# Kernel tuning notes

Measured on AMD Instinct MI355X. Metric: run time of the kernel, lower is better.

## Reference

```python
import jax, jax.numpy as jnp
import numpy as np

N_VERTICES = 100000
N_JOINTS = 24
N_BETAS = 300
PARENTS = [0, 0, 0, 0, 1, 2, 3, 4, 5, 6, 7, 8, 9, 9, 9, 12, 13, 14, 16, 17, 18, 19, 20, 21]


def rodrigues(r):
    """r: [N,1,3] axis-angle -> [N,3,3] rotation matrices.

    Original adds N(0,1e-8) noise before the norm purely to avoid 0/0; we use a
    deterministic epsilon inside the sqrt instead (same math up to ~1e-8).
    """
    theta = jnp.sqrt(jnp.sum(r * r, axis=(1, 2), keepdims=True) + 1e-16)  # [N,1,1]
    r_hat = r / theta                                                      # [N,1,3]
    cos = jnp.cos(theta)
    sin = jnp.sin(theta)
    x, y, z = r_hat[:, 0, 0], r_hat[:, 0, 1], r_hat[:, 0, 2]
    zero = jnp.zeros_like(x)
    m = jnp.stack([zero, -z, y, z, zero, -x, -y, x, zero], axis=1).reshape(-1, 3, 3)
    dot = jnp.einsum('nia,nib->nab', r_hat, r_hat)  # outer product r_hat^T r_hat
    eye = jnp.eye(3, dtype=r.dtype)
    return cos * eye + (1.0 - cos) * dot + sin * m


def _with_zeros(R3, t):
    # [3,3],[3] -> [4,4] homogeneous transform
    top = jnp.concatenate([R3, t[:, None]], axis=1)              # [3,4]
    bottom = jnp.array([[0.0, 0.0, 0.0, 1.0]], dtype=R3.dtype)
    return jnp.concatenate([top, bottom], axis=0)


def smpl_forward(beta, pose, v_template, J_regressor, skin_weights, shapedirs, posedirs):
    dtype = v_template.dtype
    # shape blendshapes: [V,3,K] . [K] -> [V,3]
    v_shaped = jnp.einsum('vdk,k->vd', shapedirs, beta) + v_template
    J = J_regressor @ v_shaped                                   # [24,3]

    pose_cube = pose.reshape(-1, 1, 3)                           # [24,1,3]
    R_cube_big = rodrigues(pose_cube)                            # [24,3,3]

    # pose blendshapes
    lrotmin = (R_cube_big[1:] - jnp.eye(3, dtype=dtype)).reshape(-1)   # [207]
    v_posed = v_shaped + jnp.einsum('vdp,p->vd', posedirs, lrotmin)    # [V,3]

    # kinematic chain (fixed 24-step sequential dependency)
    Gs = [_with_zeros(R_cube_big[0], J[0])]
    for i in range(1, N_JOINTS):
        j = PARENTS[i]
        Gs.append(Gs[j] @ _with_zeros(R_cube_big[i], J[i] - J[j]))
    G = jnp.stack(Gs)                                            # [24,4,4]

    # remove rest-pose joint locations: G - pad(G @ [J;0])
    J_h = jnp.concatenate([J, jnp.zeros((N_JOINTS, 1), dtype=dtype)], axis=1)  # [24,4]
    RJ = jnp.einsum('jab,jb->ja', G, J_h)                        # [24,4]
    G = G - jnp.pad(RJ[:, :, None], ((0, 0), (0, 0), (3, 0)))    # subtract into last column

    # linear blend skinning
    T = jnp.einsum('vj,jab->vab', skin_weights, G)               # [V,4,4]
    rest_h = jnp.pad(v_posed, ((0, 0), (0, 1)), constant_values=1.0)  # [V,4]
    v = jnp.einsum('vab,vb->va', T, rest_h)                      # [V,4]
    return v[:, :3]


def setup_inputs() -> dict:
    key = jax.random.key(0)
    ks = jax.random.split(key, 7)
    beta = jax.random.normal(ks[0], (N_BETAS,), dtype=jnp.float32)
    pose = jax.random.normal(ks[1], (N_JOINTS * 3,), dtype=jnp.float32)
    v_template = jax.random.normal(ks[2], (N_VERTICES, 3), dtype=jnp.float32)
    # NonNegUnitSum(axis=1) constraints -> nonnegative rows summing to 1
    Jr = jax.random.uniform(ks[3], (N_JOINTS, N_VERTICES), dtype=jnp.float32)
    J_regressor = Jr / jnp.sum(Jr, axis=1, keepdims=True)
    w = jax.random.uniform(ks[4], (N_VERTICES, N_JOINTS), dtype=jnp.float32)
    skin_weights = w / jnp.sum(w, axis=1, keepdims=True)
    shapedirs = 0.01 * jax.random.normal(ks[5], (N_VERTICES, 3, N_BETAS), dtype=jnp.float32)
    posedirs = 0.01 * jax.random.normal(ks[6], (N_VERTICES, 3, (N_JOINTS - 1) * 9), dtype=jnp.float32)
    return {'beta': beta, 'pose': pose, 'v_template': v_template,
            'J_regressor': J_regressor, 'skin_weights': skin_weights,
            'shapedirs': shapedirs, 'posedirs': posedirs}


def reference(beta, pose, v_template, J_regressor, skin_weights, shapedirs, posedirs):
    return smpl_forward(beta, pose, v_template, J_regressor, skin_weights, shapedirs, posedirs)
```

## Files before the change

kernel.cpp:

```cpp
#include <hip/hip_runtime.h>
#include <math.h>

#define N_V 100000
#define N_J 24
#define N_BETAS 300
#define N_POSE 207
#define JSPLIT 25

typedef float f4 __attribute__((ext_vector_type(4)));

__constant__ int c_parents[N_J] = {0,0,0,0,1,2,3,4,5,6,7,8,9,9,9,12,13,14,16,17,18,19,20,21};

__global__ void k_rodrigues(const float* __restrict__ pose,
                            float* __restrict__ ws_R,
                            float* __restrict__ ws_lrot) {
    __shared__ float Rsh[N_J][9];
    int t = threadIdx.x;
    if (t < N_J) {
        float x = pose[t*3+0], y = pose[t*3+1], z = pose[t*3+2];
        float th = sqrtf(x*x + y*y + z*z + 1e-16f);
        float inv = 1.0f / th;
        float rx = x*inv, ry = y*inv, rz = z*inv;
        float c = cosf(th), s = sinf(th), o = 1.0f - c;
        float R[9];
        R[0] = c + o*rx*rx;      R[1] = o*rx*ry - s*rz;  R[2] = o*rx*rz + s*ry;
        R[3] = o*ry*rx + s*rz;   R[4] = c + o*ry*ry;     R[5] = o*ry*rz - s*rx;
        R[6] = o*rz*rx - s*ry;   R[7] = o*rz*ry + s*rx;  R[8] = c + o*rz*rz;
        #pragma unroll
        for (int i = 0; i < 9; ++i) { Rsh[t][i] = R[i]; ws_R[t*9+i] = R[i]; }
    }
    __syncthreads();
    for (int i = t; i < N_POSE; i += blockDim.x) {
        int j = i / 9 + 1, e = i % 9;
        float v = Rsh[j][e];
        if (e == 0 || e == 4 || e == 8) v -= 1.0f;
        ws_lrot[i] = v;
    }
}

__global__ __launch_bounds__(256) void k_vertex(
        const float* __restrict__ shapedirs, const float* __restrict__ posedirs,
        const float* __restrict__ v_template, const float* __restrict__ beta,
        const float* __restrict__ lrot,
        float* __restrict__ vs, float* __restrict__ vp) {
    int lane = threadIdx.x & 63;
    int wave = threadIdx.x >> 6;
    int vb = blockIdx.x * 16 + wave * 4;

    f4 bv[4];
    #pragma unroll
    for (int it = 0; it < 4; ++it) {
        int i = lane + it * 64;
        int d = (i >= 150) ? 2 : ((i >= 75) ? 1 : 0);
        int k4 = i - d * 75;
        if (it < 3 || i < 225) bv[it] = ((const f4*)beta)[k4];
        else                   bv[it] = (f4){0.f, 0.f, 0.f, 0.f};
    }
    int f0 = 4 * lane;
    f4 lrc0 = { lrot[(f0+0)%207], lrot[(f0+1)%207], lrot[(f0+2)%207], lrot[(f0+3)%207] };
    f4 lrc1 = { lrot[(f0+256)%207], lrot[(f0+257)%207], lrot[(f0+258)%207], lrot[(f0+259)%207] };
    f4 lrc2 = { lrot[(f0+512)%207], lrot[(f0+513)%207], lrot[(f0+514)%207], lrot[(f0+515)%207] };
    float tc = lrot[206];

    #pragma unroll 2
    for (int u = 0; u < 4; ++u) {
        int v = vb + u;
        const f4*    sb = (const f4*)(shapedirs + (size_t)v * 900);
        const float* pb = posedirs + (size_t)v * 621;

        f4 s0 = __builtin_nontemporal_load(sb + lane);
        f4 s1 = __builtin_nontemporal_load(sb + lane + 64);
        f4 s2 = __builtin_nontemporal_load(sb + lane + 128);
        f4 s3 = (lane < 33) ? __builtin_nontemporal_load(sb + lane + 192)
                            : (f4){0.f, 0.f, 0.f, 0.f};
        f4 x0, x1, x2 = (f4){0.f, 0.f, 0.f, 0.f};
        __builtin_memcpy(&x0, pb + f0, 16);
        __builtin_memcpy(&x1, pb + f0 + 256, 16);
        if (lane < 27) __builtin_memcpy(&x2, pb + f0 + 512, 16);
        float tail = (lane == 27) ? pb[620] : 0.f;

        float a0 = 0.f, a1 = 0.f, a2 = 0.f;
        float p0 = 0.f, p1 = 0.f, p2 = 0.f;

        float c0 = s0.x*bv[0].x + s0.y*bv[0].y + s0.z*bv[0].z + s0.w*bv[0].w;
        float c1 = s1.x*bv[1].x + s1.y*bv[1].y + s1.z*bv[1].z + s1.w*bv[1].w;
        float c2 = s2.x*bv[2].x + s2.y*bv[2].y + s2.z*bv[2].z + s2.w*bv[2].w;
        float c3 = s3.x*bv[3].x + s3.y*bv[3].y + s3.z*bv[3].z + s3.w*bv[3].w;
        a0 += c0;
        if (lane < 11) a0 += c1; else a1 += c1;
        if (lane < 22) a1 += c2; else a2 += c2;
        a2 += c3;

        float d0 = x0.x*lrc0.x + x0.y*lrc0.y + x0.z*lrc0.z + x0.w*lrc0.w;
        float d1 = x1.x*lrc1.x + x1.y*lrc1.y + x1.z*lrc1.z + x1.w*lrc1.w;
        float d2 = x2.x*lrc2.x + x2.y*lrc2.y + x2.z*lrc2.z + x2.w*lrc2.w;
        if (lane < 51)       p0 += d0;
        else if (lane == 51) { float hi = x0.w * lrc0.w; p0 += d0 - hi; p1 += hi; }
        else                 p1 += d0;
        if (lane < 39)       p1 += d1;
        else if (lane == 39) { float hi = x1.z*lrc1.z + x1.w*lrc1.w; p1 += d1 - hi; p2 += hi; }
        else                 p2 += d1;
        p2 += d2 + tail * tc;

        #pragma unroll
        for (int off = 1; off <= 4; off <<= 1) {
            a0 += __shfl_xor(a0, off); a1 += __shfl_xor(a1, off); a2 += __shfl_xor(a2, off);
            p0 += __shfl_xor(p0, off); p1 += __shfl_xor(p1, off); p2 += __shfl_xor(p2, off);
        }
        int j = lane & 7;
        float val = a0;
        val = (j == 1) ? a1 : val;
        val = (j == 2) ? a2 : val;
        val = (j == 3) ? p0 : val;
        val = (j == 4) ? p1 : val;
        val = (j == 5) ? p2 : val;
        val += __shfl_xor(val, 8);
        val += __shfl_xor(val, 16);
        val += __shfl_xor(val, 32);
        float pj = __shfl(val, lane + 3);

        if (lane < 3) {
            float vsd = val + v_template[(size_t)v*3 + lane];
            vs[lane * N_V + v] = vsd;
            vp[lane * N_V + v] = vsd + pj;
        }
    }
}

__global__ __launch_bounds__(256) void k_jreg(const float* __restrict__ Jr,
                                              const float* __restrict__ vs,
                                              float* __restrict__ jpart) {
    int j = blockIdx.x / JSPLIT;
    int s = blockIdx.x % JSPLIT;
    const int chunk4 = (N_V / JSPLIT) / 4;
    int b4 = s * chunk4;
    int t = threadIdx.x;
    const f4* row = (const f4*)(Jr + (size_t)j * N_V);
    const f4* X = (const f4*)(vs);
    const f4* Y = (const f4*)(vs + N_V);
    const f4* Z = (const f4*)(vs + 2 * N_V);
    float a0 = 0.f, a1 = 0.f, a2 = 0.f;
    for (int i = b4 + t; i < b4 + chunk4; i += 256) {
        f4 w = row[i];
        f4 x = X[i], y = Y[i], z = Z[i];
        a0 += w.x*x.x + w.y*x.y + w.z*x.z + w.w*x.w;
        a1 += w.x*y.x + w.y*y.y + w.z*y.z + w.w*y.w;
        a2 += w.x*z.x + w.y*z.y + w.z*z.z + w.w*z.w;
    }
    #pragma unroll
    for (int off = 32; off; off >>= 1) {
        a0 += __shfl_xor(a0, off); a1 += __shfl_xor(a1, off); a2 += __shfl_xor(a2, off);
    }
    __shared__ float red[4][3];
    int wave = t >> 6, lane = t & 63;
    if (lane == 0) { red[wave][0] = a0; red[wave][1] = a1; red[wave][2] = a2; }
    __syncthreads();
    if (t == 0) {
        jpart[(j*JSPLIT+s)*3+0] = red[0][0]+red[1][0]+red[2][0]+red[3][0];
        jpart[(j*JSPLIT+s)*3+1] = red[0][1]+red[1][1]+red[2][1]+red[3][1];
        jpart[(j*JSPLIT+s)*3+2] = red[0][2]+red[1][2]+red[2][2]+red[3][2];
    }
}

__global__ __launch_bounds__(256) void k_skin(const float* __restrict__ w,
                                              const float* __restrict__ jpart,
                                              const float* __restrict__ ws_R,
                                              const float* __restrict__ vp,
                                              float* __restrict__ out) {
    __shared__ float J[N_J][3];
    __shared__ float G[N_J][16];
    __shared__ float Gp[N_J * 12];
    int t = threadIdx.x;
    if (t < N_J * 3) {
        int j = t / 3, d = t % 3;
        float s = 0.f;
        #pragma unroll
        for (int k = 0; k < JSPLIT; ++k) s += jpart[(j*JSPLIT+k)*3 + d];
        J[j][d] = s;
    }
    __syncthreads();
    if (t < 16) {
        int a = t / 4, b = t % 4;
        float g;
        if (a < 3) g = (b < 3) ? ws_R[a*3 + b] : J[0][a];
        else       g = (b == 3) ? 1.f : 0.f;
        G[0][t] = g;
    }
    __syncthreads();
    for (int i = 1; i < N_J; ++i) {
        int p = c_parents[i];
        if (t < 16) {
            int a = t / 4, b = t % 4;
            float acc = 0.f;
            #pragma unroll
            for (int k = 0; k < 4; ++k) {
                float Ak;
                if (k < 3) Ak = (b < 3) ? ws_R[i*9 + k*3 + b] : (J[i][k] - J[p][k]);
                else       Ak = (b == 3) ? 1.f : 0.f;
                acc += G[p][a*4 + k] * Ak;
            }
            G[i][t] = acc;
        }
        __syncthreads();
    }
    for (int i = t; i < N_J * 12; i += 256) {
        int j = i / 12, r = i % 12, a = r / 4, b = r % 4;
        float g = G[j][a*4 + b];
        if (b == 3)
            g -= G[j][a*4+0]*J[j][0] + G[j][a*4+1]*J[j][1] + G[j][a*4+2]*J[j][2];
        Gp[i] = g;
    }
    __syncthreads();

    int v = blockIdx.x * 256 + t;
    if (v >= N_V) return;
    float T[12];
    #pragma unroll
    for (int r = 0; r < 12; ++r) T[r] = 0.f;
    const f4* wv = (const f4*)(w + (size_t)v * 24);
    #pragma unroll
    for (int q = 0; q < 6; ++q) {
        f4 ww = __builtin_nontemporal_load(wv + q);
        float wj[4] = {ww.x, ww.y, ww.z, ww.w};
        #pragma unroll
        for (int jj = 0; jj < 4; ++jj) {
            const float* g = &Gp[(q*4 + jj) * 12];
            #pragma unroll
            for (int r = 0; r < 12; ++r) T[r] += wj[jj] * g[r];
        }
    }
    float px = vp[v], py = vp[N_V + v], pz = vp[2*N_V + v];
    out[v*3+0] = T[0]*px + T[1]*py + T[2]*pz  + T[3];
    out[v*3+1] = T[4]*px + T[5]*py + T[6]*pz  + T[7];
    out[v*3+2] = T[8]*px + T[9]*py + T[10]*pz + T[11];
}

extern "C" void kernel_launch(void* const* d_in, const int* in_sizes, int n_in,
                              void* d_out, int out_size, void* d_ws, size_t ws_size,
                              hipStream_t stream) {
    const float* beta       = (const float*)d_in[0];
    const float* pose       = (const float*)d_in[1];
    const float* v_template = (const float*)d_in[2];
    const float* Jr         = (const float*)d_in[3];
    const float* skin_w     = (const float*)d_in[4];
    const float* shapedirs  = (const float*)d_in[5];
    const float* posedirs   = (const float*)d_in[6];
    float* out = (float*)d_out;

    float* ws      = (float*)d_ws;
    float* ws_R    = ws;
    float* ws_lrot = ws + 256;
    float* ws_vs   = ws + 512;
    float* ws_vp   = ws + 512 + 3*N_V;
    float* ws_jp   = ws + 512 + 6*N_V;

    k_rodrigues<<<1, 256, 0, stream>>>(pose, ws_R, ws_lrot);
    k_vertex<<<N_V / 16, 256, 0, stream>>>(shapedirs, posedirs, v_template,
                                           beta, ws_lrot, ws_vs, ws_vp);
    k_jreg<<<N_J * JSPLIT, 256, 0, stream>>>(Jr, ws_vs, ws_jp);
    k_skin<<<(N_V + 255) / 256, 256, 0, stream>>>(skin_w, ws_jp, ws_R, ws_vp, out);
}
```

Before: 123.3 us.

## Fuse rodrigues and joint regression into vertex kernel, add partial-sum reduce

Rodrigues is now computed redundantly in each vertex block (for lrot) and in each skinning block, which removes the separate single-block launch. The joint-regressor product is fused into the vertex kernel: each block multiplies its 16 shaped vertices by the Jr columns and writes per-block partials. A small reduce kernel then sums the 6250 partials per joint coordinate. This drops the vs round trip through global memory and one launch. In exchange it adds strided Jr reads of 16 floats per joint per block, plus redundant transcendental math in every block.

```diff
diff --git a/kernel.cpp b/kernel.cpp
--- a/kernel.cpp
+++ b/kernel.cpp
@@ -5,47 +5,40 @@
 #define N_J 24
 #define N_BETAS 300
 #define N_POSE 207
-#define JSPLIT 25
+#define NBLKV (N_V / 16)
 
 typedef float f4 __attribute__((ext_vector_type(4)));
 
 __constant__ int c_parents[N_J] = {0,0,0,0,1,2,3,4,5,6,7,8,9,9,9,12,13,14,16,17,18,19,20,21};
 
-__global__ void k_rodrigues(const float* __restrict__ pose,
-                            float* __restrict__ ws_R,
-                            float* __restrict__ ws_lrot) {
-    __shared__ float Rsh[N_J][9];
-    int t = threadIdx.x;
-    if (t < N_J) {
-        float x = pose[t*3+0], y = pose[t*3+1], z = pose[t*3+2];
-        float th = sqrtf(x*x + y*y + z*z + 1e-16f);
-        float inv = 1.0f / th;
-        float rx = x*inv, ry = y*inv, rz = z*inv;
-        float c = cosf(th), s = sinf(th), o = 1.0f - c;
-        float R[9];
-        R[0] = c + o*rx*rx;      R[1] = o*rx*ry - s*rz;  R[2] = o*rx*rz + s*ry;
-        R[3] = o*ry*rx + s*rz;   R[4] = c + o*ry*ry;     R[5] = o*ry*rz - s*rx;
-        R[6] = o*rz*rx - s*ry;   R[7] = o*rz*ry + s*rx;  R[8] = c + o*rz*rz;
-        #pragma unroll
-        for (int i = 0; i < 9; ++i) { Rsh[t][i] = R[i]; ws_R[t*9+i] = R[i]; }
-    }
-    __syncthreads();
-    for (int i = t; i < N_POSE; i += blockDim.x) {
-        int j = i / 9 + 1, e = i % 9;
-        float v = Rsh[j][e];
-        if (e == 0 || e == 4 || e == 8) v -= 1.0f;
-        ws_lrot[i] = v;
-    }
+__device__ inline void rodrigues9(const float* __restrict__ pose, int j, float R[9]) {
+    float x = pose[j*3+0], y = pose[j*3+1], z = pose[j*3+2];
+    float th = sqrtf(x*x + y*y + z*z + 1e-16f);
+    float inv = 1.0f / th;
+    float rx = x*inv, ry = y*inv, rz = z*inv;
+    float c = cosf(th), s = sinf(th), o = 1.0f - c;
+    R[0] = c + o*rx*rx;      R[1] = o*rx*ry - s*rz;  R[2] = o*rx*rz + s*ry;
+    R[3] = o*ry*rx + s*rz;   R[4] = c + o*ry*ry;     R[5] = o*ry*rz - s*rx;
+    R[6] = o*rz*rx - s*ry;   R[7] = o*rz*ry + s*rx;  R[8] = c + o*rz*rz;
 }
 
 __global__ __launch_bounds__(256) void k_vertex(
         const float* __restrict__ shapedirs, const float* __restrict__ posedirs,
         const float* __restrict__ v_template, const float* __restrict__ beta,
-        const float* __restrict__ lrot,
-        float* __restrict__ vs, float* __restrict__ vp) {
-    int lane = threadIdx.x & 63;
-    int wave = threadIdx.x >> 6;
-    int vb = blockIdx.x * 16 + wave * 4;
+        const float* __restrict__ pose, const float* __restrict__ Jr,
+        float* __restrict__ vp, float* __restrict__ jpart) {
+    __shared__ float lrot_s[N_POSE];
+    __shared__ float vsh[16][3];
+    int t = threadIdx.x;
+    int lane = t & 63, wave = t >> 6;
+
+    if (t >= 1 && t < N_J) {
+        float R[9]; rodrigues9(pose, t, R);
+        #pragma unroll
+        for (int e = 0; e < 9; ++e)
+            lrot_s[(t-1)*9 + e] = R[e] - ((e==0 || e==4 || e==8) ? 1.f : 0.f);
+    }
+    __syncthreads();
 
     f4 bv[4];
     #pragma unroll
@@ -57,10 +50,12 @@
         else                   bv[it] = (f4){0.f, 0.f, 0.f, 0.f};
     }
     int f0 = 4 * lane;
-    f4 lrc0 = { lrot[(f0+0)%207], lrot[(f0+1)%207], lrot[(f0+2)%207], lrot[(f0+3)%207] };
-    f4 lrc1 = { lrot[(f0+256)%207], lrot[(f0+257)%207], lrot[(f0+258)%207], lrot[(f0+259)%207] };
-    f4 lrc2 = { lrot[(f0+512)%207], lrot[(f0+513)%207], lrot[(f0+514)%207], lrot[(f0+515)%207] };
-    float tc = lrot[206];
+    f4 lrc0 = { lrot_s[(f0+0)%207], lrot_s[(f0+1)%207], lrot_s[(f0+2)%207], lrot_s[(f0+3)%207] };
+    f4 lrc1 = { lrot_s[(f0+256)%207], lrot_s[(f0+257)%207], lrot_s[(f0+258)%207], lrot_s[(f0+259)%207] };
+    f4 lrc2 = { lrot_s[(f0+512)%207], lrot_s[(f0+513)%207], lrot_s[(f0+514)%207], lrot_s[(f0+515)%207] };
+    float tc = lrot_s[206];
+
+    int vb = blockIdx.x * 16 + wave * 4;
 
     #pragma unroll 2
     for (int u = 0; u < 4; ++u) {
@@ -121,68 +116,67 @@
 
         if (lane < 3) {
             float vsd = val + v_template[(size_t)v*3 + lane];
-            vs[lane * N_V + v] = vsd;
+            vsh[wave*4 + u][lane] = vsd;
             vp[lane * N_V + v] = vsd + pj;
         }
     }
-}
-
-__global__ __launch_bounds__(256) void k_jreg(const float* __restrict__ Jr,
-                                              const float* __restrict__ vs,
-                                              float* __restrict__ jpart) {
-    int j = blockIdx.x / JSPLIT;
-    int s = blockIdx.x % JSPLIT;
-    const int chunk4 = (N_V / JSPLIT) / 4;
-    int b4 = s * chunk4;
+    __syncthreads();
+
+    for (int idx = t; idx < N_J * 16; idx += 256) {
+        int j = idx >> 4, vi = idx & 15;
+        float w = __builtin_nontemporal_load(Jr + (size_t)j * N_V + blockIdx.x * 16 + vi);
+        float s0 = w * vsh[vi][0];
+        float s1 = w * vsh[vi][1];
+        float s2 = w * vsh[vi][2];
+        #pragma unroll
+        for (int off = 1; off <= 8; off <<= 1) {
+            s0 += __shfl_xor(s0, off); s1 += __shfl_xor(s1, off); s2 += __shfl_xor(s2, off);
+        }
+        if ((lane & 15) == 0) {
+            jpart[(size_t)(j*3+0) * NBLKV + blockIdx.x] = s0;
+            jpart[(size_t)(j*3+1) * NBLKV + blockIdx.x] = s1;
+            jpart[(size_t)(j*3+2) * NBLKV + blockIdx.x] = s2;
+        }
+    }
+}
+
+__global__ __launch_bounds__(256) void k_jreduce(const float* __restrict__ jpart,
+                                                 float* __restrict__ Jg) {
+    int c = blockIdx.x;
+    const float* col = jpart + (size_t)c * NBLKV;
     int t = threadIdx.x;
-    const f4* row = (const f4*)(Jr + (size_t)j * N_V);
-    const f4* X = (const f4*)(vs);
-    const f4* Y = (const f4*)(vs + N_V);
-    const f4* Z = (const f4*)(vs + 2 * N_V);
-    float a0 = 0.f, a1 = 0.f, a2 = 0.f;
-    for (int i = b4 + t; i < b4 + chunk4; i += 256) {
-        f4 w = row[i];
-        f4 x = X[i], y = Y[i], z = Z[i];
-        a0 += w.x*x.x + w.y*x.y + w.z*x.z + w.w*x.w;
-        a1 += w.x*y.x + w.y*y.y + w.z*y.z + w.w*y.w;
-        a2 += w.x*z.x + w.y*z.y + w.z*z.z + w.w*z.w;
-    }
-    #pragma unroll
-    for (int off = 32; off; off >>= 1) {
-        a0 += __shfl_xor(a0, off); a1 += __shfl_xor(a1, off); a2 += __shfl_xor(a2, off);
-    }
-    __shared__ float red[4][3];
+    float s = 0.f;
+    for (int i = t; i < NBLKV; i += 256) s += col[i];
+    #pragma unroll
+    for (int off = 32; off; off >>= 1) s += __shfl_xor(s, off);
+    __shared__ float red[4];
     int wave = t >> 6, lane = t & 63;
-    if (lane == 0) { red[wave][0] = a0; red[wave][1] = a1; red[wave][2] = a2; }
-    __syncthreads();
-    if (t == 0) {
-        jpart[(j*JSPLIT+s)*3+0] = red[0][0]+red[1][0]+red[2][0]+red[3][0];
-        jpart[(j*JSPLIT+s)*3+1] = red[0][1]+red[1][1]+red[2][1]+red[3][1];
-        jpart[(j*JSPLIT+s)*3+2] = red[0][2]+red[1][2]+red[2][2]+red[3][2];
-    }
+    if (lane == 0) red[wave] = s;
+    __syncthreads();
+    if (t == 0) Jg[c] = red[0] + red[1] + red[2] + red[3];
 }
 
 __global__ __launch_bounds__(256) void k_skin(const float* __restrict__ w,
-                                              const float* __restrict__ jpart,
-                                              const float* __restrict__ ws_R,
+                                              const float* __restrict__ Jg,
+                                              const float* __restrict__ pose,
                                               const float* __restrict__ vp,
                                               float* __restrict__ out) {
+    __shared__ float Rsh[N_J][9];
     __shared__ float J[N_J][3];
     __shared__ float G[N_J][16];
     __shared__ float Gp[N_J * 12];
     int t = threadIdx.x;
-    if (t < N_J * 3) {
-        int j = t / 3, d = t % 3;
-        float s = 0.f;
-        #pragma unroll
-        for (int k = 0; k < JSPLIT; ++k) s += jpart[(j*JSPLIT+k)*3 + d];
-        J[j][d] = s;
-    }
+    if (t < N_J) {
+        float R[9]; rodrigues9(pose, t, R);
+        #pragma unroll
+        for (int e = 0; e < 9; ++e) Rsh[t][e] = R[e];
+    }
+    if (t < N_J * 3) J[t/3][t%3] = Jg[t];
     __syncthreads();
     if (t < 16) {
         int a = t / 4, b = t % 4;
         float g;
-        if (a < 3) g = (b < 3) ? ws_R[a*3 + b] : J[0][a];
+        if (a < 3) g = (b < 3) ? Rsh[0][a*3 + b] : J[0][a];
         else       g = (b == 3) ? 1.f : 0.f;
         G[0][t] = g;
     }
@@ -195,7 +189,7 @@
             #pragma unroll
             for (int k = 0; k < 4; ++k) {
                 float Ak;
-                if (k < 3) Ak = (b < 3) ? ws_R[i*9 + k*3 + b] : (J[i][k] - J[p][k]);
+                if (k < 3) Ak = (b < 3) ? Rsh[i][k*3 + b] : (J[i][k] - J[p][k]);
                 else       Ak = (b == 3) ? 1.f : 0.f;
                 acc += G[p][a*4 + k] * Ak;
             }
@@ -247,16 +241,13 @@
     const float* posedirs   = (const float*)d_in[6];
     float* out = (float*)d_out;
 
-    float* ws      = (float*)d_ws;
-    float* ws_R    = ws;
-    float* ws_lrot = ws + 256;
-    float* ws_vs   = ws + 512;
-    float* ws_vp   = ws + 512 + 3*N_V;
-    float* ws_jp   = ws + 512 + 6*N_V;
-
-    k_rodrigues<<<1, 256, 0, stream>>>(pose, ws_R, ws_lrot);
-    k_vertex<<<N_V / 16, 256, 0, stream>>>(shapedirs, posedirs, v_template,
-                                           beta, ws_lrot, ws_vs, ws_vp);
-    k_jreg<<<N_J * JSPLIT, 256, 0, stream>>>(Jr, ws_vs, ws_jp);
-    k_skin<<<(N_V + 255) / 256, 256, 0, stream>>>(skin_w, ws_jp, ws_R, ws_vp, out);
-}
+    float* ws    = (float*)d_ws;
+    float* ws_vp = ws;
+    float* ws_jp = ws + 3*N_V;
+    float* ws_J  = ws + 3*N_V + 72*NBLKV;
+
+    k_vertex<<<NBLKV, 256, 0, stream>>>(shapedirs, posedirs, v_template,
+                                        beta, pose, Jr, ws_vp, ws_jp);
+    k_jreduce<<<N_J * 3, 256, 0, stream>>>(ws_jp, ws_J);
+    k_skin<<<(N_V + 255) / 256, 256, 0, stream>>>(skin_w, ws_J, pose, ws_vp, out);
+}
```

After: 127.3 us. +3.2%, slower.
